# Kernel optimization log

Measured on AMD Instinct MI355X. Metric: run time of the kernel, lower is better.

Reference implementation:

```python
import jax, jax.numpy as jnp
import numpy as np

T, B = 256, 512
IMG_FLAT = 25          # 5*5*num_channels
FEAT = 16; LOC = 4; EMB = 4
LSTM_IN = FEAT + LOC + EMB  # 24
H = 128
GRID = 10.0


def _lin(k, out_d, in_d, scale=0.05):
    kw, kb = jax.random.split(k)
    return (jax.random.normal(kw, (out_d, in_d), jnp.float32) * scale,
            jax.random.normal(kb, (out_d,), jnp.float32) * scale)


def setup_inputs() -> dict:
    key = jax.random.key(0)
    ks = jax.random.split(key, 16)
    image = jax.random.uniform(ks[0], (T * B, 5, 5), jnp.float32) * 255.0
    location = jax.random.uniform(ks[1], (T * B, 2), jnp.float32) * GRID
    message = jax.random.normal(ks[2], (T * B, 1), jnp.float32)
    done = jax.random.randint(ks[3], (T * B,), 0, 2, jnp.int32)
    h0 = jnp.zeros((1, B, H), jnp.float32)
    c0 = jnp.zeros((1, B, H), jnp.float32)
    Wv1, bv1 = _lin(ks[4], 256, IMG_FLAT)
    Wv2, bv2 = _lin(ks[5], 256, 256)
    Wv3, bv3 = _lin(ks[6], 128, 256)
    Wv4, bv4 = _lin(ks[7], FEAT, 128)
    Wl, bl = _lin(ks[8], LOC, 2)
    Wm, bm = _lin(ks[9], EMB, 1)
    Wih, bih = _lin(ks[10], 4 * H, LSTM_IN)
    Whh, bhh = _lin(ks[11], 4 * H, H)
    return dict(image=image, location=location, message=message, done=done,
                h0=h0, c0=c0,
                Wv1=Wv1, bv1=bv1, Wv2=Wv2, bv2=bv2, Wv3=Wv3, bv3=bv3,
                Wv4=Wv4, bv4=bv4, Wl=Wl, bl=bl, Wm=Wm, bm=bm,
                Wih=Wih, bih=bih, Whh=Whh, bhh=bhh)


def _get_states(image, location, message, done_f, h0, c0,
                Wv1, bv1, Wv2, bv2, Wv3, bv3, Wv4, bv4,
                Wl, bl, Wm, bm, Wih, bih, Whh, bhh):
    batch = h0.shape[1]
    # encoders (all rows at once, faithful to torch version)
    x = image.reshape(image.shape[0], -1) / 255.0
    f = jax.nn.relu(x @ Wv1.T + bv1)
    f = jax.nn.relu(f @ Wv2.T + bv2)
    f = jax.nn.relu(f @ Wv3.T + bv3)
    image_feat = jax.nn.relu(f @ Wv4.T + bv4)                  # [TB, 16]
    loc_feat = (location / GRID) @ Wl.T + bl                    # [TB, 4]
    msg = (1.0 - done_f)[:, None] * message
    msg_feat = jax.nn.relu(msg @ Wm.T + bm)                     # [TB, 4]
    hid = jnp.concatenate([image_feat, loc_feat, msg_feat], axis=1)
    hid = hid.reshape(-1, batch, LSTM_IN)                       # [T, B, 24]
    d_seq = done_f.reshape(-1, batch)                           # [T, B]

    def step(carry, xd):
        h, c = carry
        x_t, d_t = xd
        mask = (1.0 - d_t)[:, None]
        h = h * mask
        c = c * mask
        gates = x_t @ Wih.T + bih + h @ Whh.T + bhh             # [B, 4H]
        i, fg, g, o = jnp.split(gates, 4, axis=-1)
        c = jax.nn.sigmoid(fg) * c + jax.nn.sigmoid(i) * jnp.tanh(g)
        h = jax.nn.sigmoid(o) * jnp.tanh(c)
        return (h, c), h

    (hT, cT), hs = jax.lax.scan(step, (h0[0], c0[0]), (hid, d_seq))
    new_hidden = hs.reshape(-1, H)                              # [TB, 128]
    return new_hidden, hT[None], cT[None]


def reference(image, location, message, done, h0, c0,
              Wv1, bv1, Wv2, bv2, Wv3, bv3, Wv4, bv4,
              Wl, bl, Wm, bm, Wih, bih, Whh, bhh):
    done_f = done.astype(jnp.float32)
    return _get_states(image, location, message, done_f, h0, c0,
                       Wv1, bv1, Wv2, bv2, Wv3, bv3, Wv4, bv4,
                       Wl, bl, Wm, bm, Wih, bih, Whh, bhh)
```

## Files before the change

kernel.cpp:

```cpp
#include <hip/hip_runtime.h>
#include <hip/hip_bf16.h>

#define T_STEPS 256
#define BATCH   512
#define HID     128
#define TBROWS  (T_STEPS * BATCH)
#define XH_STRIDE 32

typedef short  bh8   __attribute__((ext_vector_type(8)));
typedef _Float16 h8  __attribute__((ext_vector_type(8)));
typedef float  f32x4 __attribute__((ext_vector_type(4)));

__device__ __forceinline__ unsigned short f2bf_bits(float x) {
    union { float f; unsigned int u; } a; a.f = x;
    unsigned int r = a.u + 0x7fffu + ((a.u >> 16) & 1u);
    return (unsigned short)(r >> 16);
}
__device__ __forceinline__ unsigned short f2h_bits(float x) {
    union { _Float16 h; unsigned short u; } z; z.h = (_Float16)x; return z.u;
}
__device__ __forceinline__ unsigned int pack2h(float a, float b) {
    union { _Float16 h[2]; unsigned int u; } z;
    z.h[0] = (_Float16)a; z.h[1] = (_Float16)b; return z.u;
}
__device__ __forceinline__ unsigned int pack2bf(float a, float b) {
    return (unsigned int)f2bf_bits(a) | ((unsigned int)f2bf_bits(b) << 16);
}

#if __has_builtin(__builtin_amdgcn_rcpf)
__device__ __forceinline__ float frcp(float x) { return __builtin_amdgcn_rcpf(x); }
#else
__device__ __forceinline__ float frcp(float x) { return 1.0f / x; }
#endif
#if __has_builtin(__builtin_amdgcn_exp2f)
__device__ __forceinline__ float fexp2(float x) { return __builtin_amdgcn_exp2f(x); }
#else
__device__ __forceinline__ float fexp2(float x) { return __expf(x * 0.6931471806f); }
#endif
#define LOG2E 1.442695041f
__device__ __forceinline__ float sigf(float x) {
    return frcp(1.0f + fexp2(-x * LOG2E));
}
__device__ __forceinline__ float tanh_fast(float x) {
    return fmaf(-2.0f, frcp(1.0f + fexp2(x * (2.0f * LOG2E))), 1.0f);
}

__device__ __forceinline__ void fragstore(unsigned short* dst, const float* W,
                                          int i, int NT, int Kreal) {
    const int j    = i & 7;
    const int lane = (i >> 3) & 63;
    const int ts   = i >> 9;
    const int nt   = ts % NT;
    const int ks   = ts / NT;
    const int n = nt * 16 + (lane & 15);
    const int k = ks * 32 + (lane >> 4) * 8 + j;
    dst[i] = (k < Kreal) ? f2bf_bits(W[n * Kreal + k]) : (unsigned short)0;
}

#define NE1 8192
#define NE2 65536
#define NE3 32768
#define NE4 2048
#define NWC 81920
#define NBS 512
#define PREP_TOTAL (NE1 + NE2 + NE3 + NE4 + NWC + NBS)

__global__ __launch_bounds__(256) void prep_kernel(
    const float* __restrict__ W1, const float* __restrict__ W2,
    const float* __restrict__ W3, const float* __restrict__ W4,
    const float* __restrict__ Wih, const float* __restrict__ bih,
    const float* __restrict__ Whh, const float* __restrict__ bhh,
    unsigned short* __restrict__ w1f, unsigned short* __restrict__ w2f,
    unsigned short* __restrict__ w3f, unsigned short* __restrict__ w4f,
    unsigned short* __restrict__ wcf, float* __restrict__ bsum)
{
    int i = blockIdx.x * 256 + threadIdx.x;
    if (i < NE1) { fragstore(w1f, W1, i, 16, 25); return; }
    i -= NE1;
    if (i < NE2) { fragstore(w2f, W2, i, 16, 256); return; }
    i -= NE2;
    if (i < NE3) { fragstore(w3f, W3, i, 8, 256); return; }
    i -= NE3;
    if (i < NE4) { fragstore(w4f, W4, i, 1, 128); return; }
    i -= NE4;
    if (i < NWC) {
        const int j    = i & 7;
        const int lane = (i >> 3) & 63;
        const int ts   = i >> 9;
        const int mt   = ts / 5;
        const int kt   = ts - mt * 5;
        const int m = mt * 16 + (lane & 15);
        const int k = kt * 32 + (lane >> 4) * 8 + j;
        float v = 0.0f;
        if (k < 128)      v = Whh[m * 128 + k];
        else if (k < 152) v = Wih[m * 24 + (k - 128)];
        wcf[i] = f2h_bits(v);
        return;
    }
    i -= NWC;
    if (i < NBS) bsum[i] = bih[i] + bhh[i];
}

#define ASTRIDE 264

__global__ __launch_bounds__(256) void encoder_kernel(
    const float* __restrict__ img,
    const float* __restrict__ loc,
    const float* __restrict__ msg,
    const int*   __restrict__ done,
    const float* __restrict__ B1, const float* __restrict__ B2,
    const float* __restrict__ B3, const float* __restrict__ B4,
    const float* __restrict__ Wl, const float* __restrict__ Bl,
    const float* __restrict__ Wm, const float* __restrict__ Bm,
    const unsigned short* __restrict__ w1f, const unsigned short* __restrict__ w2f,
    const unsigned short* __restrict__ w3f, const unsigned short* __restrict__ w4f,
    unsigned short* __restrict__ xcat_h)
{
    __shared__ __align__(16) unsigned short actA[4][32][ASTRIDE];
    __shared__ __align__(16) unsigned short actB[4][32][ASTRIDE];

    const int tid  = threadIdx.x;
    const int w    = tid >> 6;
    const int lane = tid & 63;
    const int n    = lane & 15;
    const int quad = lane >> 4;
    const int wrow0 = blockIdx.x * 128 + w * 32;

    if (tid < 128) {
        const int grow = blockIdx.x * 128 + tid;
        const float l0 = loc[(size_t)grow * 2 + 0] * 0.1f;
        const float l1 = loc[(size_t)grow * 2 + 1] * 0.1f;
        #pragma unroll
        for (int c = 0; c < 4; ++c)
            xcat_h[(size_t)grow * XH_STRIDE + 16 + c] =
                f2h_bits(fmaf(Wl[c * 2 + 0], l0, fmaf(Wl[c * 2 + 1], l1, Bl[c])));
        const float mm = (1.0f - (float)done[grow]) * msg[grow];
        #pragma unroll
        for (int c = 0; c < 4; ++c)
            xcat_h[(size_t)grow * XH_STRIDE + 20 + c] =
                f2h_bits(fmaxf(fmaf(Wm[c], mm, Bm[c]), 0.0f));
    }

    const f32x4 zero4 = {0.0f, 0.0f, 0.0f, 0.0f};

    {
        bh8 bimg[2];
        #pragma unroll
        for (int sg = 0; sg < 2; ++sg) {
            const size_t grow = wrow0 + sg * 16 + n;
            #pragma unroll
            for (int j = 0; j < 8; ++j) {
                const int k = quad * 8 + j;
                const float v = (k < 25) ? img[grow * 25 + k] * (1.0f / 255.0f) : 0.0f;
                bimg[sg][j] = (short)f2bf_bits(v);
            }
        }
        f32x4 a1[16][2];
        #pragma unroll
        for (int mt = 0; mt < 16; ++mt) {
            const bh8 a = *reinterpret_cast<const bh8*>(w1f + (size_t)(mt * 64 + lane) * 8);
            a1[mt][0] = __builtin_amdgcn_mfma_f32_16x16x32_bf16(a, bimg[0], zero4, 0, 0, 0);
            a1[mt][1] = __builtin_amdgcn_mfma_f32_16x16x32_bf16(a, bimg[1], zero4, 0, 0, 0);
        }
        #pragma unroll
        for (int mt = 0; mt < 16; ++mt) {
            const float4 bv = *reinterpret_cast<const float4*>(B1 + mt * 16 + quad * 4);
            #pragma unroll
            for (int sg = 0; sg < 2; ++sg) {
                const float v0 = fmaxf(a1[mt][sg][0] + bv.x, 0.0f);
                const float v1 = fmaxf(a1[mt][sg][1] + bv.y, 0.0f);
                const float v2 = fmaxf(a1[mt][sg][2] + bv.z, 0.0f);
                const float v3 = fmaxf(a1[mt][sg][3] + bv.w, 0.0f);
                uint2 pk; pk.x = pack2bf(v0, v1); pk.y = pack2bf(v2, v3);
                *reinterpret_cast<uint2*>(&actA[w][sg * 16 + n][mt * 16 + quad * 4]) = pk;
            }
        }
    }
    __syncthreads();

    {
        f32x4 a2[16][2];
        #pragma unroll
        for (int mt = 0; mt < 16; ++mt) { a2[mt][0] = zero4; a2[mt][1] = zero4; }
        #pragma unroll
        for (int kt = 0; kt < 8; ++kt) {
            const bh8 b0 = *reinterpret_cast<const bh8*>(&actA[w][n][kt * 32 + quad * 8]);
            const bh8 b1 = *reinterpret_cast<const bh8*>(&actA[w][16 + n][kt * 32 + quad * 8]);
            #pragma unroll
            for (int mt = 0; mt < 16; ++mt) {
                const bh8 a = *reinterpret_cast<const bh8*>(
                    w2f + (size_t)((kt * 16 + mt) * 64 + lane) * 8);
                a2[mt][0] = __builtin_amdgcn_mfma_f32_16x16x32_bf16(a, b0, a2[mt][0], 0, 0, 0);
                a2[mt][1] = __builtin_amdgcn_mfma_f32_16x16x32_bf16(a, b1, a2[mt][1], 0, 0, 0);
            }
        }
        #pragma unroll
        for (int mt = 0; mt < 16; ++mt) {
            const float4 bv = *reinterpret_cast<const float4*>(B2 + mt * 16 + quad * 4);
            #pragma unroll
            for (int sg = 0; sg < 2; ++sg) {
                const float v0 = fmaxf(a2[mt][sg][0] + bv.x, 0.0f);
                const float v1 = fmaxf(a2[mt][sg][1] + bv.y, 0.0f);
                const float v2 = fmaxf(a2[mt][sg][2] + bv.z, 0.0f);
                const float v3 = fmaxf(a2[mt][sg][3] + bv.w, 0.0f);
                uint2 pk; pk.x = pack2bf(v0, v1); pk.y = pack2bf(v2, v3);
                *reinterpret_cast<uint2*>(&actB[w][sg * 16 + n][mt * 16 + quad * 4]) = pk;
            }
        }
    }
    __syncthreads();

    {
        f32x4 a3[8][2];
        #pragma unroll
        for (int mt = 0; mt < 8; ++mt) { a3[mt][0] = zero4; a3[mt][1] = zero4; }
        #pragma unroll
        for (int kt = 0; kt < 8; ++kt) {
            const bh8 b0 = *reinterpret_cast<const bh8*>(&actB[w][n][kt * 32 + quad * 8]);
            const bh8 b1 = *reinterpret_cast<const bh8*>(&actB[w][16 + n][kt * 32 + quad * 8]);
            #pragma unroll
            for (int mt = 0; mt < 8; ++mt) {
                const bh8 a = *reinterpret_cast<const bh8*>(
                    w3f + (size_t)((kt * 8 + mt) * 64 + lane) * 8);
                a3[mt][0] = __builtin_amdgcn_mfma_f32_16x16x32_bf16(a, b0, a3[mt][0], 0, 0, 0);
                a3[mt][1] = __builtin_amdgcn_mfma_f32_16x16x32_bf16(a, b1, a3[mt][1], 0, 0, 0);
            }
        }
        #pragma unroll
        for (int mt = 0; mt < 8; ++mt) {
            const float4 bv = *reinterpret_cast<const float4*>(B3 + mt * 16 + quad * 4);
            #pragma unroll
            for (int sg = 0; sg < 2; ++sg) {
                const float v0 = fmaxf(a3[mt][sg][0] + bv.x, 0.0f);
                const float v1 = fmaxf(a3[mt][sg][1] + bv.y, 0.0f);
                const float v2 = fmaxf(a3[mt][sg][2] + bv.z, 0.0f);
                const float v3 = fmaxf(a3[mt][sg][3] + bv.w, 0.0f);
                uint2 pk; pk.x = pack2bf(v0, v1); pk.y = pack2bf(v2, v3);
                *reinterpret_cast<uint2*>(&actA[w][sg * 16 + n][mt * 16 + quad * 4]) = pk;
            }
        }
    }
    __syncthreads();

    {
        f32x4 a4[2] = {zero4, zero4};
        #pragma unroll
        for (int kt = 0; kt < 4; ++kt) {
            const bh8 b0 = *reinterpret_cast<const bh8*>(&actA[w][n][kt * 32 + quad * 8]);
            const bh8 b1 = *reinterpret_cast<const bh8*>(&actA[w][16 + n][kt * 32 + quad * 8]);
            const bh8 a = *reinterpret_cast<const bh8*>(w4f + (size_t)(kt * 64 + lane) * 8);
            a4[0] = __builtin_amdgcn_mfma_f32_16x16x32_bf16(a, b0, a4[0], 0, 0, 0);
            a4[1] = __builtin_amdgcn_mfma_f32_16x16x32_bf16(a, b1, a4[1], 0, 0, 0);
        }
        const float4 bv = *reinterpret_cast<const float4*>(B4 + quad * 4);
        #pragma unroll
        for (int sg = 0; sg < 2; ++sg) {
            const int grow = wrow0 + sg * 16 + n;
            const float v0 = fmaxf(a4[sg][0] + bv.x, 0.0f);
            const float v1 = fmaxf(a4[sg][1] + bv.y, 0.0f);
            const float v2 = fmaxf(a4[sg][2] + bv.z, 0.0f);
            const float v3 = fmaxf(a4[sg][3] + bv.w, 0.0f);
            uint2 pk; pk.x = pack2h(v0, v1); pk.y = pack2h(v2, v3);
            *reinterpret_cast<uint2*>(xcat_h + (size_t)grow * XH_STRIDE + quad * 4) = pk;
        }
    }
}

#define COLS 2
#define HXS 168

__global__ __launch_bounds__(512) void lstm_kernel(
    const unsigned short* __restrict__ xcat_h,
    const int*   __restrict__ done,
    const float* __restrict__ h0,
    const float* __restrict__ c0,
    const unsigned short* __restrict__ wcf,
    const float* __restrict__ bsum,
    float* __restrict__ out)
{
    __shared__ __align__(16) unsigned short hx[2][16][HXS];
    __shared__ __align__(16) float sc[8][COLS][16][4];

    const int tid  = threadIdx.x;
    const int w    = tid >> 6;
    const int lane = tid & 63;
    const int n    = lane & 15;
    const int quad = lane >> 4;
    const int bb   = blockIdx.x * COLS;

    h8 wf[4][5];
    #pragma unroll
    for (int g = 0; g < 4; ++g)
        #pragma unroll
        for (int kt = 0; kt < 5; ++kt)
            wf[g][kt] = *reinterpret_cast<const h8*>(
                wcf + (size_t)(((g * 8 + w) * 5 + kt) * 64 + lane) * 8);

    f32x4 bini[4];
    #pragma unroll
    for (int g = 0; g < 4; ++g) {
        const float4 b = *reinterpret_cast<const float4*>(bsum + g * 128 + w * 16 + quad * 4);
        bini[g] = (f32x4){b.x, b.y, b.z, b.w};
    }

    const int col   = quad & 1;
    const int ul    = lane & 15;
    const int unit  = w * 16 + ul;
    const bool owner = lane < 32;

    float c_ = 0.0f, h0v = 0.0f;
    if (owner) {
        c_  = c0[(size_t)(bb + col) * HID + unit];
        h0v = h0[(size_t)(bb + col) * HID + unit];
    }

    for (int i = tid; i < 2 * 16 * HXS / 2; i += 512)
        reinterpret_cast<unsigned int*>(hx)[i] = 0u;
    __syncthreads();

    int mc = done[bb + col];
    int mn = done[BATCH + bb + col];
    if (owner) hx[0][col][unit] = f2h_bits(h0v * (1.0f - (float)mc));
    if (tid < COLS * 12) {
        const int nl = tid / 12, kp = tid - nl * 12;
        *reinterpret_cast<unsigned int*>(&hx[0][nl][128 + 2 * kp]) =
            *reinterpret_cast<const unsigned int*>(
                xcat_h + (size_t)(bb + nl) * XH_STRIDE + 2 * kp);
    }
    __syncthreads();

    float hl = 0.0f;

    #pragma unroll 1
    for (int s = 0; s < T_STEPS; ++s) {
        const int buf = s & 1;

        h8 bf[5];
        #pragma unroll
        for (int kt = 0; kt < 5; ++kt)
            bf[kt] = *reinterpret_cast<const h8*>(&hx[buf][n][kt * 32 + quad * 8]);

        unsigned int xreg = 0;
        if (tid < COLS * 12) {
            const int nl = tid / 12, kp = tid - nl * 12;
            const int rowx = (s + 1 < T_STEPS ? s + 1 : T_STEPS - 1) * BATCH + bb + nl;
            xreg = *reinterpret_cast<const unsigned int*>(
                xcat_h + (size_t)rowx * XH_STRIDE + 2 * kp);
        }
        const int mf = done[(s + 2 < T_STEPS ? s + 2 : T_STEPS - 1) * BATCH + bb + col];

        f32x4 acc[4];
        #pragma unroll
        for (int g = 0; g < 4; ++g) acc[g] = bini[g];
        #pragma unroll
        for (int kt = 0; kt < 5; ++kt)
            #pragma unroll
            for (int g = 0; g < 4; ++g)
                acc[g] = __builtin_amdgcn_mfma_f32_16x16x32_f16(
                    wf[g][kt], bf[kt], acc[g], 0, 0, 0);

        if (n < COLS) {
            #pragma unroll
            for (int r = 0; r < 4; ++r) {
                float4 gv;
                gv.x = acc[0][r]; gv.y = acc[1][r];
                gv.z = acc[2][r]; gv.w = acc[3][r];
                *reinterpret_cast<float4*>(&sc[w][n][quad * 4 + r][0]) = gv;
            }
        }

        if (owner) {
            const float4 gv = *reinterpret_cast<const float4*>(&sc[w][col][ul][0]);
            const float mcur = 1.0f - (float)mc;
            const float mnxt = 1.0f - (float)mn;
            const float cn = sigf(gv.y) * (c_ * mcur) + sigf(gv.x) * tanh_fast(gv.z);
            const float hn = sigf(gv.w) * tanh_fast(cn);
            c_ = cn; hl = hn;
            out[(size_t)(s * BATCH + bb + col) * HID + unit] = hn;
            hx[buf ^ 1][col][unit] = f2h_bits(hn * mnxt);
        }
        if (tid < COLS * 12) {
            const int nl = tid / 12, kp = tid - nl * 12;
            *reinterpret_cast<unsigned int*>(&hx[buf ^ 1][nl][128 + 2 * kp]) = xreg;
        }
        mc = mn; mn = mf;
        __syncthreads();
    }

    const size_t base = (size_t)TBROWS * HID;
    if (owner) {
        out[base + (size_t)(bb + col) * HID + unit] = hl;
        out[base + (size_t)BATCH * HID + (size_t)(bb + col) * HID + unit] = c_;
    }
}

extern "C" void kernel_launch(void* const* d_in, const int* in_sizes, int n_in,
                              void* d_out, int out_size, void* d_ws, size_t ws_size,
                              hipStream_t stream) {
    const float* img  = (const float*)d_in[0];
    const float* loc  = (const float*)d_in[1];
    const float* msg  = (const float*)d_in[2];
    const int*   done = (const int*)d_in[3];
    const float* h0   = (const float*)d_in[4];
    const float* c0   = (const float*)d_in[5];
    const float* W1   = (const float*)d_in[6];
    const float* B1   = (const float*)d_in[7];
    const float* W2   = (const float*)d_in[8];
    const float* B2   = (const float*)d_in[9];
    const float* W3   = (const float*)d_in[10];
    const float* B3   = (const float*)d_in[11];
    const float* W4   = (const float*)d_in[12];
    const float* B4   = (const float*)d_in[13];
    const float* Wl   = (const float*)d_in[14];
    const float* Bl   = (const float*)d_in[15];
    const float* Wm   = (const float*)d_in[16];
    const float* Bm   = (const float*)d_in[17];
    const float* Wih  = (const float*)d_in[18];
    const float* bih  = (const float*)d_in[19];
    const float* Whh  = (const float*)d_in[20];
    const float* bhh  = (const float*)d_in[21];

    char* wsb = (char*)d_ws;
    unsigned short* xcat_h = (unsigned short*)wsb;
    unsigned short* w1f = (unsigned short*)(wsb + (size_t)TBROWS * XH_STRIDE * 2);
    unsigned short* w2f = w1f + NE1;
    unsigned short* w3f = w2f + NE2;
    unsigned short* w4f = w3f + NE3;
    unsigned short* wcf = w4f + NE4;
    float*          bsum = (float*)(wcf + NWC);

    float* out = (float*)d_out;

    prep_kernel<<<(PREP_TOTAL + 255) / 256, 256, 0, stream>>>(
        W1, W2, W3, W4, Wih, bih, Whh, bhh,
        w1f, w2f, w3f, w4f, wcf, bsum);
    encoder_kernel<<<TBROWS / 128, 256, 0, stream>>>(
        img, loc, msg, done, B1, B2, B3, B4, Wl, Bl, Wm, Bm,
        w1f, w2f, w3f, w4f, xcat_h);
    lstm_kernel<<<BATCH / COLS, 512, 0, stream>>>(
        xcat_h, done, h0, c0, wcf, bsum, out);
}
```

Before: 373.1 us.

## Swap MFMA operand order and redistribute gates with ds_swizzle instead of LDS

The MFMA operands are swapped so each lane's accumulator holds all four gates of one hidden unit along the batch-column dimension. A ds_swizzle replaces the per-step LDS scatter/gather through the sc buffer, removing one shared-memory round trip from the serial recurrence. The hx buffer shrinks to the two live columns, and only lanes with n<COLS load the B operand, with the rest kept at zero. This relies on the swizzle pattern and lane mapping being correct for the 16x16 MFMA output layout.

```diff
diff --git a/kernel.cpp b/kernel.cpp
--- a/kernel.cpp
+++ b/kernel.cpp
@@ -43,6 +43,11 @@
 }
 __device__ __forceinline__ float tanh_fast(float x) {
     return fmaf(-2.0f, frcp(1.0f + fexp2(x * (2.0f * LOG2E))), 1.0f);
+}
+
+__device__ __forceinline__ float swz16(float v) {
+    return __int_as_float(
+        __builtin_amdgcn_ds_swizzle(__float_as_int(v), 0x000F));
 }
 
 __device__ __forceinline__ void fragstore(unsigned short* dst, const float* W,
@@ -278,8 +283,7 @@
     const float* __restrict__ bsum,
     float* __restrict__ out)
 {
-    __shared__ __align__(16) unsigned short hx[2][16][HXS];
-    __shared__ __align__(16) float sc[8][COLS][16][4];
+    __shared__ __align__(16) unsigned short hx[2][COLS][HXS];
 
     const int tid  = threadIdx.x;
     const int w    = tid >> 6;
@@ -296,17 +300,16 @@
             wf[g][kt] = *reinterpret_cast<const h8*>(
                 wcf + (size_t)(((g * 8 + w) * 5 + kt) * 64 + lane) * 8);
 
+    const int unit = w * 16 + n;
     f32x4 bini[4];
     #pragma unroll
     for (int g = 0; g < 4; ++g) {
-        const float4 b = *reinterpret_cast<const float4*>(bsum + g * 128 + w * 16 + quad * 4);
-        bini[g] = (f32x4){b.x, b.y, b.z, b.w};
-    }
-
-    const int col   = quad & 1;
-    const int ul    = lane & 15;
-    const int unit  = w * 16 + ul;
-    const bool owner = lane < 32;
+        const float b = bsum[g * 128 + unit];
+        bini[g] = (f32x4){b, b, b, b};
+    }
+
+    const bool owner = (lane < 32);
+    const int col = quad & 1;
 
     float c_ = 0.0f, h0v = 0.0f;
     if (owner) {
@@ -314,13 +317,16 @@
         h0v = h0[(size_t)(bb + col) * HID + unit];
     }
 
-    for (int i = tid; i < 2 * 16 * HXS / 2; i += 512)
+    for (int i = tid; i < 2 * COLS * HXS / 2; i += 512)
         reinterpret_cast<unsigned int*>(hx)[i] = 0u;
     __syncthreads();
 
-    int mc = done[bb + col];
-    int mn = done[BATCH + bb + col];
-    if (owner) hx[0][col][unit] = f2h_bits(h0v * (1.0f - (float)mc));
+    int mc = 0, mn = 0;
+    if (owner) {
+        mc = done[bb + col];
+        mn = done[BATCH + bb + col];
+        hx[0][col][unit] = f2h_bits(h0v * (1.0f - (float)mc));
+    }
     if (tid < COLS * 12) {
         const int nl = tid / 12, kp = tid - nl * 12;
         *reinterpret_cast<unsigned int*>(&hx[0][nl][128 + 2 * kp]) =
@@ -331,14 +337,19 @@
 
     float hl = 0.0f;
 
+    h8 bf[5];
+    #pragma unroll
+    for (int kt = 0; kt < 5; ++kt) bf[kt] = (h8)(_Float16)0.0f;
+
     #pragma unroll 1
     for (int s = 0; s < T_STEPS; ++s) {
         const int buf = s & 1;
 
-        h8 bf[5];
-        #pragma unroll
-        for (int kt = 0; kt < 5; ++kt)
-            bf[kt] = *reinterpret_cast<const h8*>(&hx[buf][n][kt * 32 + quad * 8]);
+        if (n < COLS) {
+            #pragma unroll
+            for (int kt = 0; kt < 5; ++kt)
+                bf[kt] = *reinterpret_cast<const h8*>(&hx[buf][n][kt * 32 + quad * 8]);
+        }
 
         unsigned int xreg = 0;
         if (tid < COLS * 12) {
@@ -357,33 +368,29 @@
             #pragma unroll
             for (int g = 0; g < 4; ++g)
                 acc[g] = __builtin_amdgcn_mfma_f32_16x16x32_f16(
-                    wf[g][kt], bf[kt], acc[g], 0, 0, 0);
-
-        if (n < COLS) {
-            #pragma unroll
-            for (int r = 0; r < 4; ++r) {
-                float4 gv;
-                gv.x = acc[0][r]; gv.y = acc[1][r];
-                gv.z = acc[2][r]; gv.w = acc[3][r];
-                *reinterpret_cast<float4*>(&sc[w][n][quad * 4 + r][0]) = gv;
-            }
+                    bf[kt], wf[g][kt], acc[g], 0, 0, 0);
+
+        float g4[4];
+        #pragma unroll
+        for (int g = 0; g < 4; ++g) {
+            const float t0 = swz16(acc[g][0]);
+            const float t1 = swz16(acc[g][1]);
+            g4[g] = (lane & 16) ? t1 : t0;
         }
 
         if (owner) {
-            const float4 gv = *reinterpret_cast<const float4*>(&sc[w][col][ul][0]);
-            const float mcur = 1.0f - (float)mc;
-            const float mnxt = 1.0f - (float)mn;
-            const float cn = sigf(gv.y) * (c_ * mcur) + sigf(gv.x) * tanh_fast(gv.z);
-            const float hn = sigf(gv.w) * tanh_fast(cn);
+            const float cn = sigf(g4[1]) * (c_ * (1.0f - (float)mc))
+                           + sigf(g4[0]) * tanh_fast(g4[2]);
+            const float hn = sigf(g4[3]) * tanh_fast(cn);
             c_ = cn; hl = hn;
             out[(size_t)(s * BATCH + bb + col) * HID + unit] = hn;
-            hx[buf ^ 1][col][unit] = f2h_bits(hn * mnxt);
+            hx[buf ^ 1][col][unit] = f2h_bits(hn * (1.0f - (float)mn));
+            mc = mn; mn = mf;
         }
         if (tid < COLS * 12) {
             const int nl = tid / 12, kp = tid - nl * 12;
             *reinterpret_cast<unsigned int*>(&hx[buf ^ 1][nl][128 + 2 * kp]) = xreg;
         }
-        mc = mn; mn = mf;
         __syncthreads();
     }
 
```

New measurement: 392.4 us. 1.05x slower.
